# Optimization experiments

Measured on AMD Instinct MI355X. Metric: run time of the kernel, lower is better.

## Reference

```python
import jax, jax.numpy as jnp
import numpy as np

POOL_H, POOL_W = 7, 7


def _crop_and_resize(fm, boxes, ph, pw):
    """tf.image.crop_and_resize (bilinear) for all boxes in all batch images.

    fm: [B, H, W, C] feature map; boxes: [B, N, 4] as (y1, x1, y2, x2) in
    normalized coords. Returns [B, N, ph, pw, C].
    """
    B, H, W, C = fm.shape
    y1, x1, y2, x2 = boxes[..., 0], boxes[..., 1], boxes[..., 2], boxes[..., 3]
    ty = jnp.arange(ph, dtype=fm.dtype) / (ph - 1)               # [ph]
    tx = jnp.arange(pw, dtype=fm.dtype) / (pw - 1)               # [pw]
    # in_y = y1*(H-1) + i*(y2-y1)*(H-1)/(ph-1)  (TF crop_and_resize, crop>1)
    ys = (y1[..., None] + (y2 - y1)[..., None] * ty) * (H - 1)   # [B,N,ph]
    xs = (x1[..., None] + (x2 - x1)[..., None] * tx) * (W - 1)   # [B,N,pw]
    y0f = jnp.floor(ys)
    x0f = jnp.floor(xs)
    wy = (ys - y0f)[:, :, :, None, None]                         # [B,N,ph,1,1]
    wx = (xs - x0f)[:, :, None, :, None]                         # [B,N,1,pw,1]
    y0 = jnp.clip(y0f.astype(jnp.int32), 0, H - 1)
    y1i = jnp.clip(y0 + 1, 0, H - 1)
    x0 = jnp.clip(x0f.astype(jnp.int32), 0, W - 1)
    x1i = jnp.clip(x0 + 1, 0, W - 1)
    b = jnp.arange(B)[:, None, None, None]                        # [B,1,1,1]
    yA = y0[:, :, :, None]
    yB = y1i[:, :, :, None]                                       # [B,N,ph,1]
    xA = x0[:, :, None, :]
    xB = x1i[:, :, None, :]                                       # [B,N,1,pw]
    v00 = fm[b, yA, xA]                                           # [B,N,ph,pw,C]
    v01 = fm[b, yA, xB]
    v10 = fm[b, yB, xA]
    v11 = fm[b, yB, xB]
    top = v00 + (v01 - v00) * wx
    bot = v10 + (v11 - v10) * wx
    return top + (bot - top) * wy


def _roi_levels(boxes, image_shape):
    """FPN level assignment: clip(4 + round(log2(sqrt(h*w)*sqrt(area)/224)), 2, 5)."""
    h = boxes[..., 2] - boxes[..., 0]
    w = boxes[..., 3] - boxes[..., 1]
    image_area = (image_shape[0] * image_shape[1]).astype(jnp.float32)
    scaled_area = jnp.sqrt(h * w) * jnp.sqrt(image_area) / 224.0
    lvl = 4 + jnp.round(jnp.log2(scaled_area)).astype(jnp.int32)
    return jnp.clip(lvl, 2, 5)                                    # [B,N]


def setup_inputs():
    key = jax.random.key(0)
    kb, k2, k3, k4, k5 = jax.random.split(key, 5)
    B, N, C = 2, 1000, 256
    # valid boxes: y1 <= y2, x1 <= x2, generically nonzero area
    r = jax.random.uniform(kb, (B, N, 2, 2), dtype=jnp.float32)
    boxes = jnp.concatenate([r.min(axis=2), r.max(axis=2)], axis=-1)
    image_shape = jnp.array([1024, 1024], dtype=jnp.int32)
    p2 = jax.random.normal(k2, (B, 256, 256, C), dtype=jnp.float32)
    p3 = jax.random.normal(k3, (B, 128, 128, C), dtype=jnp.float32)
    p4 = jax.random.normal(k4, (B, 64, 64, C), dtype=jnp.float32)
    p5 = jax.random.normal(k5, (B, 32, 32, C), dtype=jnp.float32)
    return {"boxes": boxes, "image_shape": image_shape,
            "p2": p2, "p3": p3, "p4": p4, "p5": p5}


def reference(boxes, image_shape, p2, p3, p4, p5):
    # The TF layer routes each box to one pyramid level, crops there, then
    # sorts pooled features back into (batch, box) order. That composite is
    # mathematically: for each box, crop_and_resize from its assigned level.
    lvl = _roi_levels(boxes, image_shape)                         # [B,N] in {2..5}
    crop_boxes = jax.lax.stop_gradient(boxes)                     # TF stop_gradient
    pooled_all = jnp.stack(
        [_crop_and_resize(fm, crop_boxes, POOL_H, POOL_W)
         for fm in (p2, p3, p4, p5)], axis=0)                     # [4,B,N,ph,pw,C]
    idx = (lvl - 2)[None, :, :, None, None, None].astype(jnp.int32)
    idx = jnp.broadcast_to(idx, (1,) + pooled_all.shape[1:])
    return jnp.take_along_axis(pooled_all, idx, axis=0)[0]        # [B,N,ph,pw,C]
```

## Files before the change

### kernel.cpp

```cpp
#include <hip/hip_runtime.h>
#include <cmath>

#define NPOS 49

typedef float nfloat4 __attribute__((ext_vector_type(4)));

__global__ __launch_bounds__(256) void roi_align_kernel(
    const float* __restrict__ boxes,
    const int*   __restrict__ image_shape,
    const float* __restrict__ p2,
    const float* __restrict__ p3,
    const float* __restrict__ p4,
    const float* __restrict__ p5,
    float* __restrict__ out,
    int N, int C, int H2, int BN)
{
    const int gw  = blockIdx.x * 4 + (threadIdx.x >> 6);
    const int bn  = gw / NPOS;
    const int pos = gw - bn * NPOS;
    if (bn >= BN) return;

    const int b = bn / N;

    const float* bx = boxes + (size_t)bn * 4;
    const float y1 = bx[0], x1 = bx[1], y2 = bx[2], x2 = bx[3];
    const float h = y2 - y1, w = x2 - x1;

    const float img_area = (float)(image_shape[0] * image_shape[1]);
    const float scaled = sqrtf(h * w) * sqrtf(img_area) / 224.0f;
    int lvl = 4 + (int)rintf(log2f(scaled));
    lvl = min(5, max(2, lvl));

    const float* fm;
    int H;
    switch (lvl) {
        case 2:  fm = p2; H = H2;      break;
        case 3:  fm = p3; H = H2 >> 1; break;
        case 4:  fm = p4; H = H2 >> 2; break;
        default: fm = p5; H = H2 >> 3; break;
    }
    const int W = H;

    const int c = (threadIdx.x & 63) * 4;

    const float Hm1 = (float)(H - 1);
    const float Wm1 = (float)(W - 1);
    const float inv6 = 1.0f / 6.0f;

    const int py = pos / 7;
    const int px = pos - py * 7;

    const float ys = (y1 + h * ((float)py * inv6)) * Hm1;
    const float xs = (x1 + w * ((float)px * inv6)) * Wm1;
    const float y0f = floorf(ys), x0f = floorf(xs);
    const float wy = ys - y0f;
    const float wx = xs - x0f;
    int y0 = (int)y0f; y0 = min(H - 1, max(0, y0));
    int x0 = (int)x0f; x0 = min(W - 1, max(0, x0));
    const int yb = min(H - 1, y0 + 1);
    const int xb = min(W - 1, x0 + 1);

    const float* fmb = fm + (size_t)b * H * W * C;
    const float* r0 = fmb + ((size_t)y0 * W) * C;
    const float* r1 = fmb + ((size_t)yb * W) * C;

    const nfloat4 v00 = *(const nfloat4*)(r0 + (size_t)x0 * C + c);
    const nfloat4 v01 = *(const nfloat4*)(r0 + (size_t)xb * C + c);
    const nfloat4 v10 = *(const nfloat4*)(r1 + (size_t)x0 * C + c);
    const nfloat4 v11 = *(const nfloat4*)(r1 + (size_t)xb * C + c);

    const nfloat4 top = v00 + (v01 - v00) * wx;
    const nfloat4 bot = v10 + (v11 - v10) * wx;
    const nfloat4 res = top + (bot - top) * wy;

    nfloat4* dst = (nfloat4*)(out + (size_t)bn * NPOS * C + (size_t)pos * C + c);
    __builtin_nontemporal_store(res, dst);
}

extern "C" void kernel_launch(void* const* d_in, const int* in_sizes, int n_in,
                              void* d_out, int out_size, void* d_ws, size_t ws_size,
                              hipStream_t stream) {
    const float* boxes       = (const float*)d_in[0];
    const int*   image_shape = (const int*)d_in[1];
    const float* p2          = (const float*)d_in[2];
    const float* p3          = (const float*)d_in[3];
    const float* p4          = (const float*)d_in[4];
    const float* p5          = (const float*)d_in[5];
    float* out = (float*)d_out;

    const int B  = 2;
    const int BN = in_sizes[0] / 4;
    const int N  = BN / B;
    const int C  = out_size / (BN * NPOS);
    const int H2 = (int)llround(sqrt((double)in_sizes[2] / ((double)B * C)));

    const int total_waves = BN * NPOS;
    const int grid = (total_waves + 3) / 4;
    roi_align_kernel<<<grid, 256, 0, stream>>>(boxes, image_shape, p2, p3, p4, p5,
                                               out, N, C, H2, BN);
}
```

Measured before the change: 248.0 us.

## Bin boxes by pyramid level before ROI align to group feature-map accesses

Adds two preliminary kernels that compute each box's FPN level and scatter box indices into per-level lists with atomic counters in the workspace. The main kernel then walks boxes in level-sorted order, so neighbouring waves read from the same feature map, which should improve cache locality and cut divergence. This costs two extra kernel launches and an indirection load, and the order within each level is nondeterministic because of the atomics.

```diff
diff --git a/kernel.cpp b/kernel.cpp
--- a/kernel.cpp
+++ b/kernel.cpp
@@ -4,6 +4,31 @@
 #define NPOS 49
 
 typedef float nfloat4 __attribute__((ext_vector_type(4)));
+
+__device__ __forceinline__ int box_level(const float* __restrict__ bx, float img_area)
+{
+    const float h = bx[2] - bx[0], w = bx[3] - bx[1];
+    const float scaled = sqrtf(h * w) * sqrtf(img_area) / 224.0f;
+    int lvl = 4 + (int)rintf(log2f(scaled));
+    return min(5, max(2, lvl));
+}
+
+__global__ void init_counts_kernel(int* __restrict__ ws)
+{
+    if (threadIdx.x < 4) ws[threadIdx.x] = 0;
+}
+
+__global__ void bin_boxes_kernel(const float* __restrict__ boxes,
+                                 const int* __restrict__ image_shape,
+                                 int* __restrict__ ws, int BN)
+{
+    const int bn = blockIdx.x * blockDim.x + threadIdx.x;
+    if (bn >= BN) return;
+    const float img_area = (float)(image_shape[0] * image_shape[1]);
+    const int l = box_level(boxes + (size_t)bn * 4, img_area) - 2;
+    const int idx = atomicAdd(&ws[l], 1);
+    ws[4 + l * BN + idx] = bn;
+}
 
 __global__ __launch_bounds__(256) void roi_align_kernel(
     const float* __restrict__ boxes,
@@ -12,31 +37,34 @@
     const float* __restrict__ p3,
     const float* __restrict__ p4,
     const float* __restrict__ p5,
+    const int*   __restrict__ ws,
     float* __restrict__ out,
     int N, int C, int H2, int BN)
 {
-    const int gw  = blockIdx.x * 4 + (threadIdx.x >> 6);
-    const int bn  = gw / NPOS;
-    const int pos = gw - bn * NPOS;
-    if (bn >= BN) return;
+    const int gw = blockIdx.x * 4 + (threadIdx.x >> 6);
+    if (gw >= BN * NPOS) return;
+    const int box_ord = gw / NPOS;
+    const int pos     = gw - box_ord * NPOS;
 
-    const int b = bn / N;
+    const int c0 = ws[0], c1 = ws[1], c2 = ws[2];
+    int l, local;
+    if (box_ord < c0)                { l = 0; local = box_ord; }
+    else if (box_ord < c0 + c1)      { l = 1; local = box_ord - c0; }
+    else if (box_ord < c0 + c1 + c2) { l = 2; local = box_ord - c0 - c1; }
+    else                             { l = 3; local = box_ord - c0 - c1 - c2; }
+    const int bn = ws[4 + l * BN + local];
+    const int b  = bn / N;
 
     const float* bx = boxes + (size_t)bn * 4;
     const float y1 = bx[0], x1 = bx[1], y2 = bx[2], x2 = bx[3];
     const float h = y2 - y1, w = x2 - x1;
 
-    const float img_area = (float)(image_shape[0] * image_shape[1]);
-    const float scaled = sqrtf(h * w) * sqrtf(img_area) / 224.0f;
-    int lvl = 4 + (int)rintf(log2f(scaled));
-    lvl = min(5, max(2, lvl));
-
     const float* fm;
     int H;
-    switch (lvl) {
-        case 2:  fm = p2; H = H2;      break;
-        case 3:  fm = p3; H = H2 >> 1; break;
-        case 4:  fm = p4; H = H2 >> 2; break;
+    switch (l) {
+        case 0:  fm = p2; H = H2;      break;
+        case 1:  fm = p3; H = H2 >> 1; break;
+        case 2:  fm = p4; H = H2 >> 2; break;
         default: fm = p5; H = H2 >> 3; break;
     }
     const int W = H;
@@ -87,6 +115,7 @@
     const float* p4          = (const float*)d_in[4];
     const float* p5          = (const float*)d_in[5];
     float* out = (float*)d_out;
+    int*   ws  = (int*)d_ws;
 
     const int B  = 2;
     const int BN = in_sizes[0] / 4;
@@ -94,8 +123,11 @@
     const int C  = out_size / (BN * NPOS);
     const int H2 = (int)llround(sqrt((double)in_sizes[2] / ((double)B * C)));
 
+    init_counts_kernel<<<1, 64, 0, stream>>>(ws);
+    bin_boxes_kernel<<<(BN + 255) / 256, 256, 0, stream>>>(boxes, image_shape, ws, BN);
+
     const int total_waves = BN * NPOS;
     const int grid = (total_waves + 3) / 4;
     roi_align_kernel<<<grid, 256, 0, stream>>>(boxes, image_shape, p2, p3, p4, p5,
-                                               out, N, C, H2, BN);
+                                               ws, out, N, C, H2, BN);
 }
```

Measured after the change: 262.3 us. 1.06x slower.
